# Optimization experiments

Hardware: AMD Instinct MI355X
Metric: run time of the kernel (lower is better)

The kernel has to match this reference:

```python
import jax, jax.numpy as jnp
import numpy as np
import math

B, H, N, T, D, R = 1, 32, 2048, 2048, 128, 64


def setup_inputs() -> dict:
    key = jax.random.key(0)
    k1, k2, k3, k4 = jax.random.split(key, 4)
    q = jax.random.normal(k1, (B, H, N, D), dtype=jnp.float32)
    k_orig = jax.random.normal(k2, (B, H, T, D), dtype=jnp.float32)
    # emulate a quantized key: orig + small perturbation (any float tensor works)
    k_quant = k_orig + 0.05 * jax.random.normal(k3, (B, H, T, D), dtype=jnp.float32)
    # JL projection buffer: randn(dim, rank) / sqrt(rank)
    G = jax.random.normal(k4, (D, R), dtype=jnp.float32) / math.sqrt(R)
    return {"q": q, "k_orig": k_orig, "k_quant": k_quant, "G": G}


def reference(q, k_orig, k_quant, G):
    rank = G.shape[1]
    alpha = 1.0 / math.sqrt(rank)
    # compute_sign: sign of JL-projected residual -> (B,H,T,R), values in {-1,0,+1}
    e = k_orig - k_quant
    s = jnp.sign(jnp.einsum('bhtd,dr->bhtr', e, G))
    # correct_score
    raw_scores = jnp.einsum('bhnd,bhtd->bhnt', q, k_quant)          # (B,H,N,T)
    q_proj = jnp.einsum('bhnd,dr->bhnr', q, G) / math.sqrt(rank)     # (B,H,N,R)
    corr = jnp.einsum('bhnr,bhtr->bhnt', q_proj, s) * alpha          # (B,H,N,T)
    return raw_scores + corr
```

## Files before the change

kernel.cpp:

```cpp
#include <hip/hip_runtime.h>
#include <hip/hip_bf16.h>


#define H 32
#define NQ 2048
#define NT 2048
#define D 128
#define R 64
#define KDIM 192

typedef __attribute__((ext_vector_type(4))) float f32x4;
typedef __attribute__((ext_vector_type(8))) short bf16x8;

__device__ __forceinline__ void gl_lds16(const void* g, void* l) {
  __builtin_amdgcn_global_load_lds(
      (const __attribute__((address_space(1))) void*)g,
      (__attribute__((address_space(3))) void*)l, 16, 0, 0);
}

__global__ void build_kb(const float* __restrict__ ko, const float* __restrict__ kq,
                         const float* __restrict__ G, __hip_bfloat16* __restrict__ Kb) {
  __shared__ float e_sh[4][D];
  const int wave = threadIdx.x >> 6, lane = threadIdx.x & 63;
  const long row = (long)blockIdx.x * 4 + wave;
  const float* kor = ko + row * D;
  const float* kqr = kq + row * D;
  float kq0 = kqr[lane], kq1 = kqr[lane + 64];
  e_sh[wave][lane]      = kor[lane]      - kq0;
  e_sh[wave][lane + 64] = kor[lane + 64] - kq1;
  __syncthreads();
  float acc = 0.f;
  const float* e = e_sh[wave];
#pragma unroll 8
  for (int d = 0; d < D; ++d) acc += e[d] * G[d * R + lane];
  __hip_bfloat16* o = Kb + row * KDIM;
  o[lane]      = __float2bfloat16(kq0);
  o[lane + 64] = __float2bfloat16(kq1);
  float sgn = acc > 0.f ? 0.015625f : (acc < 0.f ? -0.015625f : 0.f);
  o[128 + lane] = __float2bfloat16(sgn);
}

__global__ void build_qb(const float* __restrict__ q, const float* __restrict__ G,
                         __hip_bfloat16* __restrict__ Qb) {
  __shared__ float e_sh[4][D];
  const int wave = threadIdx.x >> 6, lane = threadIdx.x & 63;
  const long row = (long)blockIdx.x * 4 + wave;
  const float* qr = q + row * D;
  float q0 = qr[lane], q1 = qr[lane + 64];
  e_sh[wave][lane]      = q0;
  e_sh[wave][lane + 64] = q1;
  __syncthreads();
  float acc = 0.f;
  const float* e = e_sh[wave];
#pragma unroll 8
  for (int d = 0; d < D; ++d) acc += e[d] * G[d * R + lane];
  __hip_bfloat16* o = Qb + row * KDIM;
  o[lane]      = __float2bfloat16(q0);
  o[lane + 64] = __float2bfloat16(q1);
  o[128 + lane] = __float2bfloat16(acc);
}

__global__ void gemm_bt(const __hip_bfloat16* __restrict__ Qb,
                        const __hip_bfloat16* __restrict__ Kb,
                        float* __restrict__ out) {
  const int h  = blockIdx.z;
  const int m0 = blockIdx.y * 128;
  const int n0 = blockIdx.x * 128;
  const __hip_bfloat16* A = Qb + (size_t)h * NQ * KDIM;
  const __hip_bfloat16* B = Kb + (size_t)h * NT * KDIM;

  __shared__ __align__(16) __hip_bfloat16 As[128 * 32];
  __shared__ __align__(16) __hip_bfloat16 Bs[128 * 32];

  const int tid = threadIdx.x, lane = tid & 63, wave = tid >> 6;
  const int wm = (wave >> 1) * 64, wn = (wave & 1) * 64;
  const int quad = lane >> 4, mrow = lane & 15;

  f32x4 acc[4][4] = {};

  const int srow = tid >> 2;
  const int scol = (tid & 3) * 8;
  const __hip_bfloat16* gA  = A + (size_t)(m0 + srow) * KDIM + scol;
  const __hip_bfloat16* gA2 = A + (size_t)(m0 + 64 + srow) * KDIM + scol;
  const __hip_bfloat16* gB  = B + (size_t)(n0 + srow) * KDIM + scol;
  const __hip_bfloat16* gB2 = B + (size_t)(n0 + 64 + srow) * KDIM + scol;
  char* lA  = (char*)As + wave * 1024;
  char* lA2 = (char*)As + 4096 + wave * 1024;
  char* lB  = (char*)Bs + wave * 1024;
  char* lB2 = (char*)Bs + 4096 + wave * 1024;

  for (int kt = 0; kt < 6; ++kt) {
    __syncthreads();
    gl_lds16(gA, lA); gl_lds16(gA2, lA2);
    gl_lds16(gB, lB); gl_lds16(gB2, lB2);
    gA += 32; gA2 += 32; gB += 32; gB2 += 32;
    __syncthreads();

    bf16x8 af[4], bfr[4];
#pragma unroll
    for (int i = 0; i < 4; ++i) {
      af[i]  = *(const bf16x8*)((const char*)As + (wm + i * 16 + mrow) * 64 + quad * 16);
      bfr[i] = *(const bf16x8*)((const char*)Bs + (wn + i * 16 + mrow) * 64 + quad * 16);
    }
#pragma unroll
    for (int i = 0; i < 4; ++i)
#pragma unroll
      for (int j = 0; j < 4; ++j)
        acc[i][j] = __builtin_amdgcn_mfma_f32_16x16x32_bf16(af[i], bfr[j], acc[i][j], 0, 0, 0);
  }

  float* orow = out + ((size_t)h * NQ + m0) * NT + n0;
#pragma unroll
  for (int i = 0; i < 4; ++i)
#pragma unroll
    for (int r = 0; r < 4; ++r) {
      const int row = wm + i * 16 + quad * 4 + r;
      float* p = orow + (size_t)row * NT + wn + mrow;
#pragma unroll
      for (int j = 0; j < 4; ++j) p[j * 16] = acc[i][j][r];
    }
}

extern "C" void kernel_launch(void* const* d_in, const int* in_sizes, int n_in,
                              void* d_out, int out_size, void* d_ws, size_t ws_size,
                              hipStream_t stream) {
  const float* q  = (const float*)d_in[0];
  const float* ko = (const float*)d_in[1];
  const float* kq = (const float*)d_in[2];
  const float* G  = (const float*)d_in[3];
  float* out = (float*)d_out;

  __hip_bfloat16* Kb = (__hip_bfloat16*)d_ws;
  __hip_bfloat16* Qb = Kb + (size_t)H * NT * KDIM;

  build_kb<<<(H * NT) / 4, 256, 0, stream>>>(ko, kq, G, Kb);
  build_qb<<<(H * NQ) / 4, 256, 0, stream>>>(q, G, Qb);

  dim3 grid(NT / 128, NQ / 128, H);
  gemm_bt<<<grid, 256, 0, stream>>>(Qb, Kb, out);
}
```

Baseline: 769.5 us.

## Fuse Q/K prep into one MFMA kernel and double-buffer GEMM LDS staging

Merges the two scalar per-row projection kernels into a single prep kernel. It computes the JL projections with bf16 MFMA, using hi/lo split-bf16 arithmetic to keep near-fp32 accuracy for the sign computation, and loads inputs with vectorized reads. The main GEMM now double-buffers its LDS tiles so the next k-slice's global-to-LDS load overlaps the current MFMAs, replacing two syncthreads per iteration with one waitcnt plus barrier. Launch bounds are added. The split-bf16 sign may still differ from fp32 near zero, and the output is dominated by the 512MB fp32 write, so gains may be limited.

New measurement: 678.6 us. -11.8%, faster.

```diff
diff --git a/kernel.cpp b/kernel.cpp
--- a/kernel.cpp
+++ b/kernel.cpp
@@ -1,5 +1,4 @@
 #include <hip/hip_runtime.h>
-#include <hip/hip_bf16.h>
 
 
 #define H 32
@@ -12,65 +11,120 @@
 typedef __attribute__((ext_vector_type(4))) float f32x4;
 typedef __attribute__((ext_vector_type(8))) short bf16x8;
 
+__device__ __forceinline__ short f2bf(float x) {
+  union { float f; unsigned u; } v; v.f = x;
+  unsigned r = v.u + 0x7fff + ((v.u >> 16) & 1);
+  return (short)(r >> 16);
+}
+__device__ __forceinline__ float bf2f(short h) {
+  union { unsigned u; float f; } v; v.u = ((unsigned)(unsigned short)h) << 16;
+  return v.f;
+}
+
 __device__ __forceinline__ void gl_lds16(const void* g, void* l) {
   __builtin_amdgcn_global_load_lds(
       (const __attribute__((address_space(1))) void*)g,
       (__attribute__((address_space(3))) void*)l, 16, 0, 0);
 }
 
-__global__ void build_kb(const float* __restrict__ ko, const float* __restrict__ kq,
-                         const float* __restrict__ G, __hip_bfloat16* __restrict__ Kb) {
-  __shared__ float e_sh[4][D];
-  const int wave = threadIdx.x >> 6, lane = threadIdx.x & 63;
-  const long row = (long)blockIdx.x * 4 + wave;
-  const float* kor = ko + row * D;
-  const float* kqr = kq + row * D;
-  float kq0 = kqr[lane], kq1 = kqr[lane + 64];
-  e_sh[wave][lane]      = kor[lane]      - kq0;
-  e_sh[wave][lane + 64] = kor[lane + 64] - kq1;
-  __syncthreads();
-  float acc = 0.f;
-  const float* e = e_sh[wave];
-#pragma unroll 8
-  for (int d = 0; d < D; ++d) acc += e[d] * G[d * R + lane];
-  __hip_bfloat16* o = Kb + row * KDIM;
-  o[lane]      = __float2bfloat16(kq0);
-  o[lane + 64] = __float2bfloat16(kq1);
-  float sgn = acc > 0.f ? 0.015625f : (acc < 0.f ? -0.015625f : 0.f);
-  o[128 + lane] = __float2bfloat16(sgn);
-}
-
-__global__ void build_qb(const float* __restrict__ q, const float* __restrict__ G,
-                         __hip_bfloat16* __restrict__ Qb) {
-  __shared__ float e_sh[4][D];
-  const int wave = threadIdx.x >> 6, lane = threadIdx.x & 63;
-  const long row = (long)blockIdx.x * 4 + wave;
-  const float* qr = q + row * D;
-  float q0 = qr[lane], q1 = qr[lane + 64];
-  e_sh[wave][lane]      = q0;
-  e_sh[wave][lane + 64] = q1;
-  __syncthreads();
-  float acc = 0.f;
-  const float* e = e_sh[wave];
-#pragma unroll 8
-  for (int d = 0; d < D; ++d) acc += e[d] * G[d * R + lane];
-  __hip_bfloat16* o = Qb + row * KDIM;
-  o[lane]      = __float2bfloat16(q0);
-  o[lane + 64] = __float2bfloat16(q1);
-  o[128 + lane] = __float2bfloat16(acc);
-}
-
-__global__ void gemm_bt(const __hip_bfloat16* __restrict__ Qb,
-                        const __hip_bfloat16* __restrict__ Kb,
-                        float* __restrict__ out) {
+__global__ __launch_bounds__(256, 2) void prep(
+    const float* __restrict__ q, const float* __restrict__ ko,
+    const float* __restrict__ kq, const float* __restrict__ G,
+    short* __restrict__ Qb, short* __restrict__ Kb) {
+  const int tid = threadIdx.x, lane = tid & 63, wave = tid >> 6;
+  const int quad = lane >> 4, mrow = lane & 15;
+  const bool kmode = blockIdx.x < (H * NT / 128);
+  const long blk = kmode ? blockIdx.x : (blockIdx.x - H * NT / 128);
+  const long rbase = blk * 128 + wave * 32;
+  short* outb = kmode ? Kb : Qb;
+
+  f32x4 acc[2][4] = {};
+
+  for (int ks = 0; ks < 4; ++ks) {
+    const int d0 = ks * 32 + quad * 8;
+    bf16x8 gh[4], gl[4];
+#pragma unroll
+    for (int j = 0; j < 4; ++j) {
+      const float* gp = G + (size_t)d0 * R + j * 16 + mrow;
+#pragma unroll
+      for (int e = 0; e < 8; ++e) {
+        float g = gp[(size_t)e * R];
+        short hb = f2bf(g);
+        gh[j][e] = hb;
+        gl[j][e] = f2bf(g - bf2f(hb));
+      }
+    }
+    bf16x8 ah[2], al[2];
+#pragma unroll
+    for (int i = 0; i < 2; ++i) {
+      const long row = rbase + i * 16 + mrow;
+      if (kmode) {
+        const f32x4 a0 = *(const f32x4*)(ko + row * D + d0);
+        const f32x4 a1 = *(const f32x4*)(ko + row * D + d0 + 4);
+        const f32x4 b0 = *(const f32x4*)(kq + row * D + d0);
+        const f32x4 b1 = *(const f32x4*)(kq + row * D + d0 + 4);
+        bf16x8 kqb;
+#pragma unroll
+        for (int t = 0; t < 4; ++t) {
+          kqb[t] = f2bf(b0[t]); kqb[t + 4] = f2bf(b1[t]);
+          float e0 = a0[t] - b0[t];
+          short h0 = f2bf(e0); ah[i][t] = h0; al[i][t] = f2bf(e0 - bf2f(h0));
+          float e1 = a1[t] - b1[t];
+          short h1 = f2bf(e1); ah[i][t + 4] = h1; al[i][t + 4] = f2bf(e1 - bf2f(h1));
+        }
+        *(bf16x8*)(Kb + row * KDIM + d0) = kqb;
+      } else {
+        const f32x4 a0 = *(const f32x4*)(q + row * D + d0);
+        const f32x4 a1 = *(const f32x4*)(q + row * D + d0 + 4);
+        bf16x8 qb;
+#pragma unroll
+        for (int t = 0; t < 4; ++t) {
+          short h0 = f2bf(a0[t]); qb[t] = h0; ah[i][t] = h0; al[i][t] = 0;
+          short h1 = f2bf(a1[t]); qb[t + 4] = h1; ah[i][t + 4] = h1; al[i][t + 4] = 0;
+        }
+        *(bf16x8*)(Qb + row * KDIM + d0) = qb;
+      }
+    }
+#pragma unroll
+    for (int i = 0; i < 2; ++i)
+#pragma unroll
+      for (int j = 0; j < 4; ++j) {
+        acc[i][j] = __builtin_amdgcn_mfma_f32_16x16x32_bf16(ah[i], gh[j], acc[i][j], 0, 0, 0);
+        if (kmode) {
+          acc[i][j] = __builtin_amdgcn_mfma_f32_16x16x32_bf16(al[i], gh[j], acc[i][j], 0, 0, 0);
+          acc[i][j] = __builtin_amdgcn_mfma_f32_16x16x32_bf16(ah[i], gl[j], acc[i][j], 0, 0, 0);
+        }
+      }
+  }
+#pragma unroll
+  for (int i = 0; i < 2; ++i)
+#pragma unroll
+    for (int j = 0; j < 4; ++j)
+#pragma unroll
+      for (int r = 0; r < 4; ++r) {
+        const long row = rbase + i * 16 + quad * 4 + r;
+        const int col = j * 16 + mrow;
+        float v = acc[i][j][r];
+        short s;
+        if (kmode)
+          s = v > 0.f ? (short)0x3C80 : (v < 0.f ? (short)0xBC80 : (short)0);
+        else
+          s = f2bf(v);
+        outb[row * KDIM + 128 + col] = s;
+      }
+}
+
+__global__ __launch_bounds__(256, 3) void gemm_bt(const short* __restrict__ Qb,
+                                                  const short* __restrict__ Kb,
+                                                  float* __restrict__ out) {
   const int h  = blockIdx.z;
   const int m0 = blockIdx.y * 128;
   const int n0 = blockIdx.x * 128;
-  const __hip_bfloat16* A = Qb + (size_t)h * NQ * KDIM;
-  const __hip_bfloat16* B = Kb + (size_t)h * NT * KDIM;
-
-  __shared__ __align__(16) __hip_bfloat16 As[128 * 32];
-  __shared__ __align__(16) __hip_bfloat16 Bs[128 * 32];
+  const short* A = Qb + (size_t)h * NQ * KDIM;
+  const short* B = Kb + (size_t)h * NT * KDIM;
+
+  __shared__ __align__(16) short As[2][128 * 32];
+  __shared__ __align__(16) short Bs[2][128 * 32];
 
   const int tid = threadIdx.x, lane = tid & 63, wave = tid >> 6;
   const int wm = (wave >> 1) * 64, wn = (wave & 1) * 64;
@@ -80,33 +134,47 @@
 
   const int srow = tid >> 2;
   const int scol = (tid & 3) * 8;
-  const __hip_bfloat16* gA  = A + (size_t)(m0 + srow) * KDIM + scol;
-  const __hip_bfloat16* gA2 = A + (size_t)(m0 + 64 + srow) * KDIM + scol;
-  const __hip_bfloat16* gB  = B + (size_t)(n0 + srow) * KDIM + scol;
-  const __hip_bfloat16* gB2 = B + (size_t)(n0 + 64 + srow) * KDIM + scol;
-  char* lA  = (char*)As + wave * 1024;
-  char* lA2 = (char*)As + 4096 + wave * 1024;
-  char* lB  = (char*)Bs + wave * 1024;
-  char* lB2 = (char*)Bs + 4096 + wave * 1024;
-
+  const short* gA  = A + (size_t)(m0 + srow) * KDIM + scol;
+  const short* gA2 = A + (size_t)(m0 + 64 + srow) * KDIM + scol;
+  const short* gB  = B + (size_t)(n0 + srow) * KDIM + scol;
+  const short* gB2 = B + (size_t)(n0 + 64 + srow) * KDIM + scol;
+
+  auto stage = [&](int b, int kt) {
+    char* a1 = (char*)(&As[b][0]) + wave * 1024;
+    char* a2 = (char*)(&As[b][0]) + 4096 + wave * 1024;
+    char* b1 = (char*)(&Bs[b][0]) + wave * 1024;
+    char* b2 = (char*)(&Bs[b][0]) + 4096 + wave * 1024;
+    gl_lds16(gA + kt * 32, a1);
+    gl_lds16(gA2 + kt * 32, a2);
+    gl_lds16(gB + kt * 32, b1);
+    gl_lds16(gB2 + kt * 32, b2);
+  };
+
+  stage(0, 0);
+  asm volatile("s_waitcnt vmcnt(0)" ::: "memory");
+  __builtin_amdgcn_s_barrier();
+
+#pragma unroll
   for (int kt = 0; kt < 6; ++kt) {
-    __syncthreads();
-    gl_lds16(gA, lA); gl_lds16(gA2, lA2);
-    gl_lds16(gB, lB); gl_lds16(gB2, lB2);
-    gA += 32; gA2 += 32; gB += 32; gB2 += 32;
-    __syncthreads();
-
-    bf16x8 af[4], bfr[4];
+    const int cur = kt & 1;
+    if (kt < 5) stage(cur ^ 1, kt + 1);
+
+    bf16x8 af[4], bfv[4];
 #pragma unroll
     for (int i = 0; i < 4; ++i) {
-      af[i]  = *(const bf16x8*)((const char*)As + (wm + i * 16 + mrow) * 64 + quad * 16);
-      bfr[i] = *(const bf16x8*)((const char*)Bs + (wn + i * 16 + mrow) * 64 + quad * 16);
+      af[i]  = *(const bf16x8*)((const char*)(&As[cur][0]) + (wm + i * 16 + mrow) * 64 + quad * 16);
+      bfv[i] = *(const bf16x8*)((const char*)(&Bs[cur][0]) + (wn + i * 16 + mrow) * 64 + quad * 16);
     }
 #pragma unroll
     for (int i = 0; i < 4; ++i)
 #pragma unroll
       for (int j = 0; j < 4; ++j)
-        acc[i][j] = __builtin_amdgcn_mfma_f32_16x16x32_bf16(af[i], bfr[j], acc[i][j], 0, 0, 0);
+        acc[i][j] = __builtin_amdgcn_mfma_f32_16x16x32_bf16(af[i], bfv[j], acc[i][j], 0, 0, 0);
+
+    if (kt < 5) {
+      asm volatile("s_waitcnt vmcnt(0)" ::: "memory");
+      __builtin_amdgcn_s_barrier();
+    }
   }
 
   float* orow = out + ((size_t)h * NQ + m0) * NT + n0;
@@ -130,11 +198,10 @@
   const float* G  = (const float*)d_in[3];
   float* out = (float*)d_out;
 
-  __hip_bfloat16* Kb = (__hip_bfloat16*)d_ws;
-  __hip_bfloat16* Qb = Kb + (size_t)H * NT * KDIM;
-
-  build_kb<<<(H * NT) / 4, 256, 0, stream>>>(ko, kq, G, Kb);
-  build_qb<<<(H * NQ) / 4, 256, 0, stream>>>(q, G, Qb);
+  short* Kb = (short*)d_ws;
+  short* Qb = Kb + (size_t)H * NT * KDIM;
+
+  prep<<<(H * NT + H * NQ) / 128, 256, 0, stream>>>(q, ko, kq, G, Qb, Kb);
 
   dim3 grid(NT / 128, NQ / 128, H);
   gemm_bt<<<grid, 256, 0, stream>>>(Qb, Kb, out);
```
